# Kernel optimization log

Measured on AMD Instinct MI355X. Metric: run time of the kernel, lower is better.

Reference implementation:

```python
import jax, jax.numpy as jnp
import numpy as np

B, S, D, E, TOPK = 8, 4096, 1024, 64, 2
TEMP = 0.01


def setup_inputs() -> dict:
    key = jax.random.key(0)
    k_x, k_w1, k_b1, k_w2, k_b2 = jax.random.split(key, 5)
    x = jax.random.normal(k_x, (B, S, D), dtype=jnp.float32)
    # torch.nn.Linear default init ~ U(-1/sqrt(fan_in), 1/sqrt(fan_in)); scale ok for reference
    W1 = jax.random.normal(k_w1, (D, 2 * D), dtype=jnp.float32) * (1.0 / np.sqrt(D))
    b1 = jax.random.normal(k_b1, (2 * D,), dtype=jnp.float32) * 0.01
    W2 = jax.random.normal(k_w2, (2 * D, E), dtype=jnp.float32) * (1.0 / np.sqrt(2 * D))
    b2 = jax.random.normal(k_b2, (E,), dtype=jnp.float32) * 0.01
    return {"x": x, "W1": W1, "b1": b1, "W2": W2, "b2": b2}


def reference(x, W1, b1, W2, b2):
    # 2-layer MLP router: [B,S,D] -> [B,S,2D] -> [B,S,E]
    h = jax.nn.relu(jnp.einsum('bsd,df->bsf', x, W1) + b1)
    logits = jnp.einsum('bsf,fe->bse', h, W2) + b2
    # top-k over experts
    top_k_logits, indices = jax.lax.top_k(logits, TOPK)  # [B,S,K]
    # scatter top-k logits into a -inf-filled tensor: equivalent to masking,
    # since scattered values equal logits at those positions
    keep = jax.nn.one_hot(indices, E, dtype=bool).any(axis=-2)  # [B,S,E]
    sparse_logits = jnp.where(keep, logits, -jnp.inf)
    router_output = jax.nn.softmax(sparse_logits, axis=-1)
    ori_router_output = jax.nn.softmax(logits / TEMP, axis=-1)
    return (ori_router_output, router_output, indices)
```

## Files before the change

kernel.cpp:

```cpp
#include <hip/hip_runtime.h>
#include <math.h>
#include <stdint.h>

#define M_TOK 32768
#define D_IN  1024
#define F_HID 2048
#define E_EXP 64

#define O_ORI 0
#define O_RTR (M_TOK * E_EXP)
#define O_IDX (2 * M_TOK * E_EXP)

typedef _Float16 half8 __attribute__((ext_vector_type(8)));
typedef float    f32x4 __attribute__((ext_vector_type(4)));
typedef unsigned int uint32;
typedef uint32   u32x4 __attribute__((ext_vector_type(4)));

#define WS_XH  ((size_t)0)
#define WS_XL  (WS_XH  + (size_t)M_TOK * D_IN * 2)
#define WS_W1H (WS_XL  + (size_t)M_TOK * D_IN * 2)
#define WS_W1L (WS_W1H + (size_t)D_IN * F_HID * 2)
#define WS_W2H (WS_W1L + (size_t)D_IN * F_HID * 2)
#define WS_W2L (WS_W2H + (size_t)F_HID * E_EXP * 2)
#define WS_P   (WS_W2L + (size_t)F_HID * E_EXP * 2)
#define WS_NEED_FULL (WS_P + (size_t)8 * M_TOK * E_EXP * 4)

__device__ __forceinline__ void split_sc(float v, float sc, unsigned short& h, unsigned short& l) {
    const _Float16 hh = (_Float16)v;
    const float hf = (float)hh;
    const _Float16 hs = (_Float16)(hf * sc);
    const _Float16 ls = (_Float16)((v - hf) * sc);
    h = __builtin_bit_cast(unsigned short, hs);
    l = __builtin_bit_cast(unsigned short, ls);
}


__global__ void split_x_k(const float* __restrict__ x,
                          unsigned short* __restrict__ xh, unsigned short* __restrict__ xl) {
    size_t i = ((size_t)blockIdx.x * 256 + threadIdx.x) * 4;
    const float4 v = *(const float4*)&x[i];
    ushort4 h, l;
    split_sc(v.x, 64.f, h.x, l.x); split_sc(v.y, 64.f, h.y, l.y);
    split_sc(v.z, 64.f, h.z, l.z); split_sc(v.w, 64.f, h.w, l.w);
    *(ushort4*)&xh[i] = h;
    *(ushort4*)&xl[i] = l;
}

__global__ void split_w1t_k(const float* __restrict__ W1,
                            unsigned short* __restrict__ wh, unsigned short* __restrict__ wl) {
    __shared__ float t[32][33];
    const int d0 = blockIdx.x * 32;
    const int f0 = blockIdx.y * 32;
    const int r  = threadIdx.x >> 3;
    const int c4 = (threadIdx.x & 7) * 4;
    const float4 v = *(const float4*)&W1[(size_t)(d0 + r) * F_HID + f0 + c4];
    t[r][c4 + 0] = v.x; t[r][c4 + 1] = v.y; t[r][c4 + 2] = v.z; t[r][c4 + 3] = v.w;
    __syncthreads();
    ushort4 h, l;
    split_sc(t[c4 + 0][r], 64.f, h.x, l.x);
    split_sc(t[c4 + 1][r], 64.f, h.y, l.y);
    split_sc(t[c4 + 2][r], 64.f, h.z, l.z);
    split_sc(t[c4 + 3][r], 64.f, h.w, l.w);
    *(ushort4*)&wh[(size_t)(f0 + r) * D_IN + d0 + c4] = h;
    *(ushort4*)&wl[(size_t)(f0 + r) * D_IN + d0 + c4] = l;
}

__global__ void split_w2f_k(const float* __restrict__ W2,
                            unsigned short* __restrict__ wh, unsigned short* __restrict__ wl) {
    const int s  = blockIdx.x;
    const int nt = threadIdx.x >> 6;
    const int l  = threadIdx.x & 63;
    const int fb = s * 32 + (l >> 4) * 8;
    const int e  = nt * 16 + (l & 15);
    unsigned short h[8], lo[8];
#pragma unroll
    for (int j = 0; j < 8; ++j)
        split_sc(W2[(size_t)(fb + j) * E_EXP + e], 16.f, h[j], lo[j]);
    const size_t base = ((size_t)(s * 4 + nt) * 64 + l) * 8;
    ((ushort4*)&wh[base])[0] = make_ushort4(h[0], h[1], h[2], h[3]);
    ((ushort4*)&wh[base])[1] = make_ushort4(h[4], h[5], h[6], h[7]);
    ((ushort4*)&wl[base])[0] = make_ushort4(lo[0], lo[1], lo[2], lo[3]);
    ((ushort4*)&wl[base])[1] = make_ushort4(lo[4], lo[5], lo[6], lo[7]);
}


__device__ __forceinline__ uint32 swz(uint32 o) { return o ^ (((o >> 7) & 7u) << 4); }

#define STAGE16(SRCP, DSTP) \
    __builtin_amdgcn_global_load_lds((const __attribute__((address_space(1))) void*)(SRCP), \
                                     (__attribute__((address_space(3))) void*)(DSTP), 16, 0, 0)


__launch_bounds__(512, 2)
__global__ void gemm1_8w(const unsigned short* __restrict__ xh, const unsigned short* __restrict__ xl,
                         const unsigned short* __restrict__ w1h, const unsigned short* __restrict__ w1l,
                         const unsigned short* __restrict__ w2fh, const unsigned short* __restrict__ w2fl,
                         const float* __restrict__ b1,
                         float* __restrict__ partials)
{
    __shared__ __align__(16) unsigned char lds[131072];

    const int tid  = threadIdx.x;
    const int lane = tid & 63;
    const int w    = tid >> 6;
    const int c15  = lane & 15;
    const int g    = lane >> 4;
    const int wr   = w >> 2;
    const int wc   = w & 3;

    const int bid  = blockIdx.x;
    const int fblk = bid & 7;
    const int mblk = bid >> 3;
    const size_t tok0 = (size_t)mblk * 128;
    const int f0 = fblk * 256;

    uint32 arow, ahalf, brow[2], bhalf[2];
    {
        const uint32 sA = swz((uint32)(tid * 16));
        arow = sA >> 6; ahalf = (sA & 63u) >> 1;
#pragma unroll
        for (int j = 0; j < 2; ++j) {
            const uint32 sB = swz((uint32)(j * 8192 + w * 1024 + lane * 16));
            brow[j] = sB >> 6; bhalf[j] = (sB & 63u) >> 1;
        }
    }

    uint32 offA[4], offB[4];
#pragma unroll
    for (int m = 0; m < 4; ++m)
        offA[m] = swz((uint32)((wr * 64 + m * 16 + c15) * 64 + g * 16));
#pragma unroll
    for (int n = 0; n < 4; ++n)
        offB[n] = swz((uint32)((wc * 64 + n * 16 + c15) * 64 + g * 16));

    f32x4 acc[4][4];
#pragma unroll
    for (int m = 0; m < 4; ++m)
#pragma unroll
        for (int n = 0; n < 4; ++n) acc[m][n] = (f32x4){0.f, 0.f, 0.f, 0.f};

#define STAGE_T(T, BUF) do {                                                         \
    const int d0_ = (T) * 32;                                                        \
    const size_t asrc = (tok0 + arow) * D_IN + (size_t)(d0_ + (int)ahalf);           \
    STAGE16(xh + asrc, lds + (BUF) * 16384 + w * 1024);                              \
    STAGE16(xl + asrc, lds + (BUF) * 16384 + 8192 + w * 1024);                       \
    _Pragma("unroll")                                                                \
    for (int j = 0; j < 2; ++j) {                                                    \
        const size_t bsrc = ((size_t)f0 + brow[j]) * D_IN + (size_t)(d0_ + (int)bhalf[j]); \
        STAGE16(w1h + bsrc, lds + 32768 + (BUF) * 32768 + j * 8192 + w * 1024);      \
        STAGE16(w1l + bsrc, lds + 32768 + (BUF) * 32768 + 16384 + j * 8192 + w * 1024); \
    } } while (0)

    STAGE_T(0, 0);
    STAGE_T(1, 1);

#pragma unroll 1
    for (int t = 0; t < 32; ++t) {
        if (t < 31) asm volatile("s_waitcnt vmcnt(6)" ::: "memory");
        else        asm volatile("s_waitcnt vmcnt(0)" ::: "memory");
        __builtin_amdgcn_s_barrier();
        const unsigned char* Ab = lds + (t & 1) * 16384;
        const unsigned char* Bb = lds + 32768 + (t & 1) * 32768;

        half8 b1f[4], b2f[4];
#pragma unroll
        for (int n = 0; n < 4; ++n) {
            b1f[n] = *(const half8*)(Bb + offB[n]);
            b2f[n] = *(const half8*)(Bb + 16384 + offB[n]);
        }
        half8 a1f[2], a2f[2];
#pragma unroll
        for (int m = 0; m < 2; ++m) {
            a1f[m] = *(const half8*)(Ab + offA[m]);
            a2f[m] = *(const half8*)(Ab + 8192 + offA[m]);
        }
        __builtin_amdgcn_s_setprio(1);
#pragma unroll
        for (int m = 0; m < 2; ++m)
#pragma unroll
            for (int n = 0; n < 4; ++n) {
                acc[m][n] = __builtin_amdgcn_mfma_f32_16x16x32_f16(a1f[m], b1f[n], acc[m][n], 0, 0, 0);
                acc[m][n] = __builtin_amdgcn_mfma_f32_16x16x32_f16(a1f[m], b2f[n], acc[m][n], 0, 0, 0);
                acc[m][n] = __builtin_amdgcn_mfma_f32_16x16x32_f16(a2f[m], b1f[n], acc[m][n], 0, 0, 0);
            }
        __builtin_amdgcn_s_setprio(0);
#pragma unroll
        for (int m = 0; m < 2; ++m) {
            a1f[m] = *(const half8*)(Ab + offA[2 + m]);
            a2f[m] = *(const half8*)(Ab + 8192 + offA[2 + m]);
        }
        __builtin_amdgcn_s_setprio(1);
#pragma unroll
        for (int m = 0; m < 2; ++m)
#pragma unroll
            for (int n = 0; n < 4; ++n) {
                acc[2 + m][n] = __builtin_amdgcn_mfma_f32_16x16x32_f16(a1f[m], b1f[n], acc[2 + m][n], 0, 0, 0);
                acc[2 + m][n] = __builtin_amdgcn_mfma_f32_16x16x32_f16(a1f[m], b2f[n], acc[2 + m][n], 0, 0, 0);
                acc[2 + m][n] = __builtin_amdgcn_mfma_f32_16x16x32_f16(a2f[m], b1f[n], acc[2 + m][n], 0, 0, 0);
            }
        __builtin_amdgcn_s_setprio(0);
        __builtin_amdgcn_s_barrier();
        if (t + 2 < 32) STAGE_T(t + 2, t & 1);
    }
#undef STAGE_T

    {
        float bv[4];
#pragma unroll
        for (int n = 0; n < 4; ++n) bv[n] = b1[f0 + wc * 64 + n * 16 + c15];
#pragma unroll
        for (int m = 0; m < 4; ++m)
#pragma unroll
            for (int n = 0; n < 4; ++n)
#pragma unroll
                for (int r = 0; r < 4; ++r) {
                    float hv = acc[m][n][r] * (1.f / 4096.f) + bv[n];
                    hv = fmaxf(hv, 0.f);
                    const _Float16 hh = (_Float16)hv;
                    const float hf = (float)hh;
                    const _Float16 hsv = (_Float16)(hf * 16.f);
                    const _Float16 lsv = (_Float16)((hv - hf) * 16.f);
                    const uint32 pk = (uint32)__builtin_bit_cast(unsigned short, hsv)
                                    | ((uint32)__builtin_bit_cast(unsigned short, lsv) << 16);
                    const int tok = wr * 64 + m * 16 + g * 4 + r;
                    const int fl  = wc * 64 + n * 16 + c15;
                    *(uint32*)(lds + tok * 1024 + ((fl * 4) ^ ((tok & 15) << 4))) = pk;
                }
    }
    __syncthreads();

    f32x4 acc2[4];
#pragma unroll
    for (int nt = 0; nt < 4; ++nt) acc2[nt] = (f32x4){0.f, 0.f, 0.f, 0.f};

    const int wtok0 = w * 16;
    const int tokA  = wtok0 + c15;
#pragma unroll
    for (int s = 0; s < 8; ++s) {
        const int kf = s * 32 + g * 8;
        const int sg = fblk * 8 + s;
        half8 bf1[4], bf2[4];
#pragma unroll
        for (int nt = 0; nt < 4; ++nt) {
            const size_t base = ((size_t)(sg * 4 + nt) * 64 + lane) * 8;
            bf1[nt] = *(const half8*)&w2fh[base];
            bf2[nt] = *(const half8*)&w2fl[base];
        }
        const u32x4 q0 = *(const u32x4*)(lds + tokA * 1024 + (((kf    ) * 4) ^ (c15 << 4)));
        const u32x4 q1 = *(const u32x4*)(lds + tokA * 1024 + (((kf + 4) * 4) ^ (c15 << 4)));
        u32x4 hi4, lo4;
        hi4[0] = __builtin_amdgcn_perm(q0[1], q0[0], 0x05040100u);
        hi4[1] = __builtin_amdgcn_perm(q0[3], q0[2], 0x05040100u);
        hi4[2] = __builtin_amdgcn_perm(q1[1], q1[0], 0x05040100u);
        hi4[3] = __builtin_amdgcn_perm(q1[3], q1[2], 0x05040100u);
        lo4[0] = __builtin_amdgcn_perm(q0[1], q0[0], 0x07060302u);
        lo4[1] = __builtin_amdgcn_perm(q0[3], q0[2], 0x07060302u);
        lo4[2] = __builtin_amdgcn_perm(q1[1], q1[0], 0x07060302u);
        lo4[3] = __builtin_amdgcn_perm(q1[3], q1[2], 0x07060302u);
        const half8 a1 = __builtin_bit_cast(half8, hi4);
        const half8 a2 = __builtin_bit_cast(half8, lo4);
#pragma unroll
        for (int nt = 0; nt < 4; ++nt) {
            acc2[nt] = __builtin_amdgcn_mfma_f32_16x16x32_f16(a1, bf1[nt], acc2[nt], 0, 0, 0);
            acc2[nt] = __builtin_amdgcn_mfma_f32_16x16x32_f16(a1, bf2[nt], acc2[nt], 0, 0, 0);
            acc2[nt] = __builtin_amdgcn_mfma_f32_16x16x32_f16(a2, bf1[nt], acc2[nt], 0, 0, 0);
        }
    }

    float* pout = partials + ((size_t)fblk * M_TOK + tok0) * E_EXP;
#pragma unroll
    for (int nt = 0; nt < 4; ++nt)
#pragma unroll
        for (int r = 0; r < 4; ++r) {
            const int tl = wtok0 + g * 4 + r;
            pout[(size_t)tl * E_EXP + nt * 16 + c15] = acc2[nt][r] * (1.f / 256.f);
        }
}


__launch_bounds__(256, 4)
__global__ void finalize(const float* __restrict__ partials,
                         const float* __restrict__ b2,
                         float* __restrict__ out)
{
    const int lane = threadIdx.x & 63;
    const int w    = threadIdx.x >> 6;
    const size_t tok0 = (size_t)blockIdx.x * 64;
    const int e = lane;
    const float be = b2[e];

#pragma unroll 1
    for (int i = 0; i < 16; ++i) {
        const size_t tok = tok0 + (size_t)w * 16 + i;
        float l = be;
#pragma unroll
        for (int p = 0; p < 8; ++p)
            l += partials[((size_t)p * M_TOK + tok) * E_EXP + e];

        float v = l; int idx = e;
#pragma unroll
        for (int m = 32; m >= 1; m >>= 1) {
            const float ov = __shfl_xor(v, m, 64);
            const int   oi = __shfl_xor(idx, m, 64);
            if (ov > v || (ov == v && oi < idx)) { v = ov; idx = oi; }
        }
        const float m1 = v; const int i1 = idx;

        v = (e == i1) ? -INFINITY : l; idx = e;
#pragma unroll
        for (int m = 32; m >= 1; m >>= 1) {
            const float ov = __shfl_xor(v, m, 64);
            const int   oi = __shfl_xor(idx, m, 64);
            if (ov > v || (ov == v && oi < idx)) { v = ov; idx = oi; }
        }
        const int i2 = idx;

        const float ex = expf((l - m1) * 100.0f);
        float s = ex;
#pragma unroll
        for (int m = 32; m >= 1; m >>= 1) s += __shfl_xor(s, m, 64);
        const float ori = ex / s;

        const float q = (e == i1 || e == i2) ? expf(l - m1) : 0.f;
        float s2 = q;
#pragma unroll
        for (int m = 32; m >= 1; m >>= 1) s2 += __shfl_xor(s2, m, 64);
        const float rtr = q / s2;

        out[O_ORI + tok * E_EXP + e] = ori;
        out[O_RTR + tok * E_EXP + e] = rtr;
        if (e == 0) {
            out[O_IDX + tok * 2 + 0] = (float)i1;
            out[O_IDX + tok * 2 + 1] = (float)i2;
        }
    }
}


#define BT  64
#define NB  256

__launch_bounds__(256, 2)
__global__ void router_mfma(const unsigned short* __restrict__ xh, const unsigned short* __restrict__ xl,
                            const unsigned short* __restrict__ w1h, const unsigned short* __restrict__ w1l,
                            const unsigned short* __restrict__ w2fh, const unsigned short* __restrict__ w2fl,
                            const float* __restrict__ b1, const float* __restrict__ b2,
                            float* __restrict__ out)
{
    __shared__ __align__(16) unsigned char xs_h[BT * 64];
    __shared__ __align__(16) unsigned char xs_l[BT * 64];
    __shared__ __align__(16) unsigned char w1s_h[NB * 64];
    __shared__ __align__(16) unsigned char w1s_l[NB * 64];
    __shared__ __align__(16) unsigned char hsbuf[BT * 132 * 4];

    const int tid  = threadIdx.x;
    const int lane = tid & 63;
    const int w    = tid >> 6;
    const int c15  = lane & 15;
    const int g    = lane >> 4;
    const size_t tok0 = (size_t)blockIdx.x * BT;

    uint32* hs = (uint32*)hsbuf;
    float*  ls = (float*)hsbuf;

    f32x4 acc2h[4], acc2x[4];
#pragma unroll
    for (int nt = 0; nt < 4; ++nt) {
        acc2h[nt] = (f32x4){0.f, 0.f, 0.f, 0.f};
        acc2x[nt] = (f32x4){0.f, 0.f, 0.f, 0.f};
    }

    const uint32 kqb = (uint32)g * 16u;

    for (int fc = 0; fc < F_HID; fc += NB) {
        f32x4 ahh[4][4], axx[4][4];
#pragma unroll
        for (int mt = 0; mt < 4; ++mt)
#pragma unroll
            for (int nt = 0; nt < 4; ++nt) {
                ahh[mt][nt] = (f32x4){0.f, 0.f, 0.f, 0.f};
                axx[mt][nt] = (f32x4){0.f, 0.f, 0.f, 0.f};
            }

        for (int d0 = 0; d0 < D_IN; d0 += 32) {
            __syncthreads();
            {
                uint32 o = (uint32)w * 1024u + (uint32)lane * 16u;
                uint32 s = swz(o);
                uint32 r = s >> 6, hb = (s & 63u) >> 1;
                const unsigned short* sp;
                sp = xh + (tok0 + r) * D_IN + (size_t)(d0 + (int)hb);
                STAGE16(sp, xs_h + (size_t)w * 1024);
                sp = xl + (tok0 + r) * D_IN + (size_t)(d0 + (int)hb);
                STAGE16(sp, xs_l + (size_t)w * 1024);
#pragma unroll
                for (int q = 0; q < 4; ++q) {
                    const uint32 c_ = (uint32)(q * 4 + w);
                    uint32 o2 = c_ * 1024u + (uint32)lane * 16u;
                    uint32 s2 = swz(o2);
                    uint32 r2 = s2 >> 6, hb2 = (s2 & 63u) >> 1;
                    sp = w1h + ((size_t)(fc + (int)r2)) * D_IN + (size_t)(d0 + (int)hb2);
                    STAGE16(sp, w1s_h + (size_t)c_ * 1024);
                    sp = w1l + ((size_t)(fc + (int)r2)) * D_IN + (size_t)(d0 + (int)hb2);
                    STAGE16(sp, w1s_l + (size_t)c_ * 1024);
                }
            }
            __syncthreads();

            half8 ah[4], al[4], bh[4], bl[4];
#pragma unroll
            for (int mt = 0; mt < 4; ++mt) {
                const uint32 off = swz((uint32)(mt * 16 + c15) * 64u + kqb);
                ah[mt] = *(const half8*)(xs_h + off);
                al[mt] = *(const half8*)(xs_l + off);
            }
#pragma unroll
            for (int nt = 0; nt < 4; ++nt) {
                const uint32 row = (uint32)(w * 64 + nt * 16 + c15);
                const uint32 off = swz(row * 64u + kqb);
                bh[nt] = *(const half8*)(w1s_h + off);
                bl[nt] = *(const half8*)(w1s_l + off);
            }
#pragma unroll
            for (int mt = 0; mt < 4; ++mt)
#pragma unroll
                for (int nt = 0; nt < 4; ++nt) {
                    ahh[mt][nt] = __builtin_amdgcn_mfma_f32_16x16x32_f16(ah[mt], bh[nt], ahh[mt][nt], 0, 0, 0);
                    axx[mt][nt] = __builtin_amdgcn_mfma_f32_16x16x32_f16(ah[mt], bl[nt], axx[mt][nt], 0, 0, 0);
                    axx[mt][nt] = __builtin_amdgcn_mfma_f32_16x16x32_f16(al[mt], bh[nt], axx[mt][nt], 0, 0, 0);
                }
        }

        const int fl0 = (w & 1) * 64;
#pragma unroll
        for (int phase = 0; phase < 2; ++phase) {
            if ((w >> 1) == phase) {
#pragma unroll
                for (int nt = 0; nt < 4; ++nt) {
                    const float b1v = b1[fc + w * 64 + nt * 16 + c15];
#pragma unroll
                    for (int mt = 0; mt < 4; ++mt) {
#pragma unroll
                        for (int r = 0; r < 4; ++r) {
                            float hv = (ahh[mt][nt][r] + axx[mt][nt][r]) * (1.f / 4096.f) + b1v;
                            hv = fmaxf(hv, 0.f);
                            const _Float16 hhv0 = (_Float16)hv;
                            const float hf = (float)hhv0;
                            const _Float16 hhv = (_Float16)(hf * 16.f);
                            const _Float16 hlv = (_Float16)((hv - hf) * 16.f);
                            uint32 pk = (uint32)__builtin_bit_cast(unsigned short, hhv)
                                      | ((uint32)__builtin_bit_cast(unsigned short, hlv) << 16);
                            const int t = mt * 16 + g * 4 + r;
                            hs[t * 132 + fl0 + nt * 16 + c15] = pk;
                        }
                    }
                }
            }
            __syncthreads();
            const int tA = w * 16 + c15;
#pragma unroll
            for (int ktl = 0; ktl < 4; ++ktl) {
                const u32x4 q0 = *(const u32x4*)&hs[tA * 132 + ktl * 32 + g * 8];
                const u32x4 q1 = *(const u32x4*)&hs[tA * 132 + ktl * 32 + g * 8 + 4];
                u32x4 hi4, lo4;
                hi4[0] = __builtin_amdgcn_perm(q0[1], q0[0], 0x05040100u);
                hi4[1] = __builtin_amdgcn_perm(q0[3], q0[2], 0x05040100u);
                hi4[2] = __builtin_amdgcn_perm(q1[1], q1[0], 0x05040100u);
                hi4[3] = __builtin_amdgcn_perm(q1[3], q1[2], 0x05040100u);
                lo4[0] = __builtin_amdgcn_perm(q0[1], q0[0], 0x07060302u);
                lo4[1] = __builtin_amdgcn_perm(q0[3], q0[2], 0x07060302u);
                lo4[2] = __builtin_amdgcn_perm(q1[1], q1[0], 0x07060302u);
                lo4[3] = __builtin_amdgcn_perm(q1[3], q1[2], 0x07060302u);
                const half8 a_h = __builtin_bit_cast(half8, hi4);
                const half8 a_l = __builtin_bit_cast(half8, lo4);
                const int sg = (fc >> 5) + phase * 4 + ktl;
#pragma unroll
                for (int nt = 0; nt < 4; ++nt) {
                    const size_t base = ((size_t)(sg * 4 + nt) * 64 + lane) * 8;
                    const half8 b_h = *(const half8*)&w2fh[base];
                    const half8 b_l = *(const half8*)&w2fl[base];
                    acc2h[nt] = __builtin_amdgcn_mfma_f32_16x16x32_f16(a_h, b_h, acc2h[nt], 0, 0, 0);
                    acc2x[nt] = __builtin_amdgcn_mfma_f32_16x16x32_f16(a_h, b_l, acc2x[nt], 0, 0, 0);
                    acc2x[nt] = __builtin_amdgcn_mfma_f32_16x16x32_f16(a_l, b_h, acc2x[nt], 0, 0, 0);
                }
            }
            __syncthreads();
        }
    }

#pragma unroll
    for (int nt = 0; nt < 4; ++nt)
#pragma unroll
        for (int r = 0; r < 4; ++r) {
            const int t = w * 16 + g * 4 + r;
            ls[t * 68 + nt * 16 + c15] = (acc2h[nt][r] + acc2x[nt][r]) * (1.f / 256.f);
        }
    __syncthreads();

    const int e = lane;
    const float be = b2[e];
#pragma unroll 1
    for (int i = 0; i < 16; ++i) {
        const float l = ls[(w * 16 + i) * 68 + e] + be;

        float v = l; int idx = e;
#pragma unroll
        for (int m = 32; m >= 1; m >>= 1) {
            const float ov = __shfl_xor(v, m, 64);
            const int   oi = __shfl_xor(idx, m, 64);
            if (ov > v || (ov == v && oi < idx)) { v = ov; idx = oi; }
        }
        const float m1 = v; const int i1 = idx;

        v = (e == i1) ? -INFINITY : l; idx = e;
#pragma unroll
        for (int m = 32; m >= 1; m >>= 1) {
            const float ov = __shfl_xor(v, m, 64);
            const int   oi = __shfl_xor(idx, m, 64);
            if (ov > v || (ov == v && oi < idx)) { v = ov; idx = oi; }
        }
        const int i2 = idx;

        const float ex = expf((l - m1) * 100.0f);
        float s = ex;
#pragma unroll
        for (int m = 32; m >= 1; m >>= 1) s += __shfl_xor(s, m, 64);
        const float ori = ex / s;

        const float q = (e == i1 || e == i2) ? expf(l - m1) : 0.f;
        float s2 = q;
#pragma unroll
        for (int m = 32; m >= 1; m >>= 1) s2 += __shfl_xor(s2, m, 64);
        const float rtr = q / s2;

        const size_t tok = tok0 + (size_t)w * 16 + i;
        out[O_ORI + tok * E_EXP + e] = ori;
        out[O_RTR + tok * E_EXP + e] = rtr;
        if (e == 0) {
            out[O_IDX + tok * 2 + 0] = (float)i1;
            out[O_IDX + tok * 2 + 1] = (float)i2;
        }
    }
}


extern "C" void kernel_launch(void* const* d_in, const int* in_sizes, int n_in,
                              void* d_out, int out_size, void* d_ws, size_t ws_size,
                              hipStream_t stream) {
    const float* x  = (const float*)d_in[0];
    const float* W1 = (const float*)d_in[1];
    const float* b1 = (const float*)d_in[2];
    const float* W2 = (const float*)d_in[3];
    const float* b2 = (const float*)d_in[4];
    float* out = (float*)d_out;

    unsigned char* ws = (unsigned char*)d_ws;
    unsigned short* xh  = (unsigned short*)(ws + WS_XH);
    unsigned short* xl  = (unsigned short*)(ws + WS_XL);
    unsigned short* w1h = (unsigned short*)(ws + WS_W1H);
    unsigned short* w1l = (unsigned short*)(ws + WS_W1L);
    unsigned short* w2h = (unsigned short*)(ws + WS_W2H);
    unsigned short* w2l = (unsigned short*)(ws + WS_W2L);
    float*          parts = (float*)(ws + WS_P);

    hipLaunchKernelGGL(split_x_k,  dim3(M_TOK * D_IN / 4 / 256), dim3(256), 0, stream, x, xh, xl);
    hipLaunchKernelGGL(split_w1t_k, dim3(D_IN / 32, F_HID / 32), dim3(256), 0, stream, W1, w1h, w1l);
    hipLaunchKernelGGL(split_w2f_k, dim3(F_HID / 32), dim3(256), 0, stream, W2, w2h, w2l);

    if (ws_size >= WS_NEED_FULL) {
        hipLaunchKernelGGL(gemm1_8w, dim3(2048), dim3(512), 0, stream,
                           xh, xl, w1h, w1l, w2h, w2l, b1, parts);
        hipLaunchKernelGGL(finalize, dim3(M_TOK / 64), dim3(256), 0, stream, parts, b2, out);
    } else {
        hipLaunchKernelGGL(router_mfma, dim3(M_TOK / BT), dim3(256), 0, stream,
                           xh, xl, w1h, w1l, w2h, w2l, b1, b2, out);
    }
}
```

Before: 524.3 us.

## Fuse both router GEMMs and the softmax finalize into one kernel

Each block now owns 128 tokens and loops over all eight 256-wide hidden chunks. For each chunk it runs the first GEMM, writes the ReLU hidden tile into LDS, and accumulates the second GEMM in registers. The top-k and softmax epilogue then runs in the same kernel from an LDS logits tile. This removes the 8-way partial-logit buffer in global memory (a large write and read) and the separate finalize launch. The cost is a grid of only 256 large blocks, with the hidden-tile conversion and second GEMM serialized inside each block between chunks, which limits latency hiding.

```diff
diff --git a/kernel.cpp b/kernel.cpp
--- a/kernel.cpp
+++ b/kernel.cpp
@@ -22,8 +22,7 @@
 #define WS_W1L (WS_W1H + (size_t)D_IN * F_HID * 2)
 #define WS_W2H (WS_W1L + (size_t)D_IN * F_HID * 2)
 #define WS_W2L (WS_W2H + (size_t)F_HID * E_EXP * 2)
-#define WS_P   (WS_W2L + (size_t)F_HID * E_EXP * 2)
-#define WS_NEED_FULL (WS_P + (size_t)8 * M_TOK * E_EXP * 4)
+#define WS_NEED (WS_W2L + (size_t)F_HID * E_EXP * 2)
 
 __device__ __forceinline__ void split_sc(float v, float sc, unsigned short& h, unsigned short& l) {
     const _Float16 hh = (_Float16)v;
@@ -92,11 +91,11 @@
 
 
 __launch_bounds__(512, 2)
-__global__ void gemm1_8w(const unsigned short* __restrict__ xh, const unsigned short* __restrict__ xl,
-                         const unsigned short* __restrict__ w1h, const unsigned short* __restrict__ w1l,
-                         const unsigned short* __restrict__ w2fh, const unsigned short* __restrict__ w2fl,
-                         const float* __restrict__ b1,
-                         float* __restrict__ partials)
+__global__ void router_one(const unsigned short* __restrict__ xh, const unsigned short* __restrict__ xl,
+                           const unsigned short* __restrict__ w1h, const unsigned short* __restrict__ w1l,
+                           const unsigned short* __restrict__ w2fh, const unsigned short* __restrict__ w2fl,
+                           const float* __restrict__ b1, const float* __restrict__ b2,
+                           float* __restrict__ out)
 {
     __shared__ __align__(16) unsigned char lds[131072];
 
@@ -108,11 +107,7 @@
     const int wr   = w >> 2;
     const int wc   = w & 3;
 
-    const int bid  = blockIdx.x;
-    const int fblk = bid & 7;
-    const int mblk = bid >> 3;
-    const size_t tok0 = (size_t)mblk * 128;
-    const int f0 = fblk * 256;
+    const size_t tok0 = (size_t)blockIdx.x * 128;
 
     uint32 arow, ahalf, brow[2], bhalf[2];
     {
@@ -133,169 +128,161 @@
     for (int n = 0; n < 4; ++n)
         offB[n] = swz((uint32)((wc * 64 + n * 16 + c15) * 64 + g * 16));
 
-    f32x4 acc[4][4];
-#pragma unroll
-    for (int m = 0; m < 4; ++m)
-#pragma unroll
-        for (int n = 0; n < 4; ++n) acc[m][n] = (f32x4){0.f, 0.f, 0.f, 0.f};
-
-#define STAGE_T(T, BUF) do {                                                         \
+    f32x4 acc2[4];
+#pragma unroll
+    for (int nt = 0; nt < 4; ++nt) acc2[nt] = (f32x4){0.f, 0.f, 0.f, 0.f};
+
+#define STAGE_T(T, BUF, F0) do {                                                     \
     const int d0_ = (T) * 32;                                                        \
     const size_t asrc = (tok0 + arow) * D_IN + (size_t)(d0_ + (int)ahalf);           \
     STAGE16(xh + asrc, lds + (BUF) * 16384 + w * 1024);                              \
     STAGE16(xl + asrc, lds + (BUF) * 16384 + 8192 + w * 1024);                       \
     _Pragma("unroll")                                                                \
     for (int j = 0; j < 2; ++j) {                                                    \
-        const size_t bsrc = ((size_t)f0 + brow[j]) * D_IN + (size_t)(d0_ + (int)bhalf[j]); \
+        const size_t bsrc = ((size_t)(F0) + brow[j]) * D_IN + (size_t)(d0_ + (int)bhalf[j]); \
         STAGE16(w1h + bsrc, lds + 32768 + (BUF) * 32768 + j * 8192 + w * 1024);      \
         STAGE16(w1l + bsrc, lds + 32768 + (BUF) * 32768 + 16384 + j * 8192 + w * 1024); \
     } } while (0)
 
-    STAGE_T(0, 0);
-    STAGE_T(1, 1);
-
 #pragma unroll 1
-    for (int t = 0; t < 32; ++t) {
-        if (t < 31) asm volatile("s_waitcnt vmcnt(6)" ::: "memory");
-        else        asm volatile("s_waitcnt vmcnt(0)" ::: "memory");
-        __builtin_amdgcn_s_barrier();
-        const unsigned char* Ab = lds + (t & 1) * 16384;
-        const unsigned char* Bb = lds + 32768 + (t & 1) * 32768;
-
-        half8 b1f[4], b2f[4];
-#pragma unroll
-        for (int n = 0; n < 4; ++n) {
-            b1f[n] = *(const half8*)(Bb + offB[n]);
-            b2f[n] = *(const half8*)(Bb + 16384 + offB[n]);
-        }
-        half8 a1f[2], a2f[2];
-#pragma unroll
-        for (int m = 0; m < 2; ++m) {
-            a1f[m] = *(const half8*)(Ab + offA[m]);
-            a2f[m] = *(const half8*)(Ab + 8192 + offA[m]);
-        }
-        __builtin_amdgcn_s_setprio(1);
-#pragma unroll
-        for (int m = 0; m < 2; ++m)
+    for (int fc = 0; fc < F_HID; fc += 256) {
+        f32x4 acc[4][4];
+#pragma unroll
+        for (int m = 0; m < 4; ++m)
+#pragma unroll
+            for (int n = 0; n < 4; ++n) acc[m][n] = (f32x4){0.f, 0.f, 0.f, 0.f};
+
+        __syncthreads();
+        STAGE_T(0, 0, fc);
+        STAGE_T(1, 1, fc);
+
+#pragma unroll 1
+        for (int t = 0; t < 32; ++t) {
+            if (t < 31) asm volatile("s_waitcnt vmcnt(6)" ::: "memory");
+            else        asm volatile("s_waitcnt vmcnt(0)" ::: "memory");
+            __builtin_amdgcn_s_barrier();
+            const unsigned char* Ab = lds + (t & 1) * 16384;
+            const unsigned char* Bb = lds + 32768 + (t & 1) * 32768;
+
+            half8 b1f[4], b2f[4];
 #pragma unroll
             for (int n = 0; n < 4; ++n) {
-                acc[m][n] = __builtin_amdgcn_mfma_f32_16x16x32_f16(a1f[m], b1f[n], acc[m][n], 0, 0, 0);
-                acc[m][n] = __builtin_amdgcn_mfma_f32_16x16x32_f16(a1f[m], b2f[n], acc[m][n], 0, 0, 0);
-                acc[m][n] = __builtin_amdgcn_mfma_f32_16x16x32_f16(a2f[m], b1f[n], acc[m][n], 0, 0, 0);
-            }
-        __builtin_amdgcn_s_setprio(0);
-#pragma unroll
-        for (int m = 0; m < 2; ++m) {
-            a1f[m] = *(const half8*)(Ab + offA[2 + m]);
-            a2f[m] = *(const half8*)(Ab + 8192 + offA[2 + m]);
-        }
-        __builtin_amdgcn_s_setprio(1);
-#pragma unroll
-        for (int m = 0; m < 2; ++m)
-#pragma unroll
-            for (int n = 0; n < 4; ++n) {
-                acc[2 + m][n] = __builtin_amdgcn_mfma_f32_16x16x32_f16(a1f[m], b1f[n], acc[2 + m][n], 0, 0, 0);
-                acc[2 + m][n] = __builtin_amdgcn_mfma_f32_16x16x32_f16(a1f[m], b2f[n], acc[2 + m][n], 0, 0, 0);
-                acc[2 + m][n] = __builtin_amdgcn_mfma_f32_16x16x32_f16(a2f[m], b1f[n], acc[2 + m][n], 0, 0, 0);
-            }
-        __builtin_amdgcn_s_setprio(0);
-        __builtin_amdgcn_s_barrier();
-        if (t + 2 < 32) STAGE_T(t + 2, t & 1);
+                b1f[n] = *(const half8*)(Bb + offB[n]);
+                b2f[n] = *(const half8*)(Bb + 16384 + offB[n]);
+            }
+            half8 a1f[2], a2f[2];
+#pragma unroll
+            for (int m = 0; m < 2; ++m) {
+                a1f[m] = *(const half8*)(Ab + offA[m]);
+                a2f[m] = *(const half8*)(Ab + 8192 + offA[m]);
+            }
+            __builtin_amdgcn_s_setprio(1);
+#pragma unroll
+            for (int m = 0; m < 2; ++m)
+#pragma unroll
+                for (int n = 0; n < 4; ++n) {
+                    acc[m][n] = __builtin_amdgcn_mfma_f32_16x16x32_f16(a1f[m], b1f[n], acc[m][n], 0, 0, 0);
+                    acc[m][n] = __builtin_amdgcn_mfma_f32_16x16x32_f16(a1f[m], b2f[n], acc[m][n], 0, 0, 0);
+                    acc[m][n] = __builtin_amdgcn_mfma_f32_16x16x32_f16(a2f[m], b1f[n], acc[m][n], 0, 0, 0);
+                }
+            __builtin_amdgcn_s_setprio(0);
+#pragma unroll
+            for (int m = 0; m < 2; ++m) {
+                a1f[m] = *(const half8*)(Ab + offA[2 + m]);
+                a2f[m] = *(const half8*)(Ab + 8192 + offA[2 + m]);
+            }
+            __builtin_amdgcn_s_setprio(1);
+#pragma unroll
+            for (int m = 0; m < 2; ++m)
+#pragma unroll
+                for (int n = 0; n < 4; ++n) {
+                    acc[2 + m][n] = __builtin_amdgcn_mfma_f32_16x16x32_f16(a1f[m], b1f[n], acc[2 + m][n], 0, 0, 0);
+                    acc[2 + m][n] = __builtin_amdgcn_mfma_f32_16x16x32_f16(a1f[m], b2f[n], acc[2 + m][n], 0, 0, 0);
+                    acc[2 + m][n] = __builtin_amdgcn_mfma_f32_16x16x32_f16(a2f[m], b1f[n], acc[2 + m][n], 0, 0, 0);
+                }
+            __builtin_amdgcn_s_setprio(0);
+            __builtin_amdgcn_s_barrier();
+            if (t + 2 < 32) STAGE_T(t + 2, t & 1, fc);
+        }
+
+        {
+            float bv[4];
+#pragma unroll
+            for (int n = 0; n < 4; ++n) bv[n] = b1[fc + wc * 64 + n * 16 + c15];
+#pragma unroll
+            for (int m = 0; m < 4; ++m)
+#pragma unroll
+                for (int n = 0; n < 4; ++n)
+#pragma unroll
+                    for (int r = 0; r < 4; ++r) {
+                        float hv = acc[m][n][r] * (1.f / 4096.f) + bv[n];
+                        hv = fmaxf(hv, 0.f);
+                        const _Float16 hh = (_Float16)hv;
+                        const float hf = (float)hh;
+                        const _Float16 hsv = (_Float16)(hf * 16.f);
+                        const _Float16 lsv = (_Float16)((hv - hf) * 16.f);
+                        const uint32 pk = (uint32)__builtin_bit_cast(unsigned short, hsv)
+                                        | ((uint32)__builtin_bit_cast(unsigned short, lsv) << 16);
+                        const int tok = wr * 64 + m * 16 + g * 4 + r;
+                        const int fl  = wc * 64 + n * 16 + c15;
+                        *(uint32*)(lds + tok * 1024 + ((fl * 4) ^ ((tok & 15) << 4))) = pk;
+                    }
+        }
+        __syncthreads();
+
+        {
+            const int tokA = w * 16 + c15;
+#pragma unroll
+            for (int s = 0; s < 8; ++s) {
+                const int kf = s * 32 + g * 8;
+                const int sg = (fc >> 5) + s;
+                half8 bf1[4], bf2[4];
+#pragma unroll
+                for (int nt = 0; nt < 4; ++nt) {
+                    const size_t base = ((size_t)(sg * 4 + nt) * 64 + lane) * 8;
+                    bf1[nt] = *(const half8*)&w2fh[base];
+                    bf2[nt] = *(const half8*)&w2fl[base];
+                }
+                const u32x4 q0 = *(const u32x4*)(lds + tokA * 1024 + (((kf    ) * 4) ^ (c15 << 4)));
+                const u32x4 q1 = *(const u32x4*)(lds + tokA * 1024 + (((kf + 4) * 4) ^ (c15 << 4)));
+                u32x4 hi4, lo4;
+                hi4[0] = __builtin_amdgcn_perm(q0[1], q0[0], 0x05040100u);
+                hi4[1] = __builtin_amdgcn_perm(q0[3], q0[2], 0x05040100u);
+                hi4[2] = __builtin_amdgcn_perm(q1[1], q1[0], 0x05040100u);
+                hi4[3] = __builtin_amdgcn_perm(q1[3], q1[2], 0x05040100u);
+                lo4[0] = __builtin_amdgcn_perm(q0[1], q0[0], 0x07060302u);
+                lo4[1] = __builtin_amdgcn_perm(q0[3], q0[2], 0x07060302u);
+                lo4[2] = __builtin_amdgcn_perm(q1[1], q1[0], 0x07060302u);
+                lo4[3] = __builtin_amdgcn_perm(q1[3], q1[2], 0x07060302u);
+                const half8 a1 = __builtin_bit_cast(half8, hi4);
+                const half8 a2 = __builtin_bit_cast(half8, lo4);
+#pragma unroll
+                for (int nt = 0; nt < 4; ++nt) {
+                    acc2[nt] = __builtin_amdgcn_mfma_f32_16x16x32_f16(a1, bf1[nt], acc2[nt], 0, 0, 0);
+                    acc2[nt] = __builtin_amdgcn_mfma_f32_16x16x32_f16(a1, bf2[nt], acc2[nt], 0, 0, 0);
+                    acc2[nt] = __builtin_amdgcn_mfma_f32_16x16x32_f16(a2, bf1[nt], acc2[nt], 0, 0, 0);
+                }
+            }
+        }
     }
 #undef STAGE_T
 
-    {
-        float bv[4];
-#pragma unroll
-        for (int n = 0; n < 4; ++n) bv[n] = b1[f0 + wc * 64 + n * 16 + c15];
-#pragma unroll
-        for (int m = 0; m < 4; ++m)
-#pragma unroll
-            for (int n = 0; n < 4; ++n)
-#pragma unroll
-                for (int r = 0; r < 4; ++r) {
-                    float hv = acc[m][n][r] * (1.f / 4096.f) + bv[n];
-                    hv = fmaxf(hv, 0.f);
-                    const _Float16 hh = (_Float16)hv;
-                    const float hf = (float)hh;
-                    const _Float16 hsv = (_Float16)(hf * 16.f);
-                    const _Float16 lsv = (_Float16)((hv - hf) * 16.f);
-                    const uint32 pk = (uint32)__builtin_bit_cast(unsigned short, hsv)
-                                    | ((uint32)__builtin_bit_cast(unsigned short, lsv) << 16);
-                    const int tok = wr * 64 + m * 16 + g * 4 + r;
-                    const int fl  = wc * 64 + n * 16 + c15;
-                    *(uint32*)(lds + tok * 1024 + ((fl * 4) ^ ((tok & 15) << 4))) = pk;
-                }
-    }
     __syncthreads();
-
-    f32x4 acc2[4];
-#pragma unroll
-    for (int nt = 0; nt < 4; ++nt) acc2[nt] = (f32x4){0.f, 0.f, 0.f, 0.f};
-
-    const int wtok0 = w * 16;
-    const int tokA  = wtok0 + c15;
-#pragma unroll
-    for (int s = 0; s < 8; ++s) {
-        const int kf = s * 32 + g * 8;
-        const int sg = fblk * 8 + s;
-        half8 bf1[4], bf2[4];
-#pragma unroll
-        for (int nt = 0; nt < 4; ++nt) {
-            const size_t base = ((size_t)(sg * 4 + nt) * 64 + lane) * 8;
-            bf1[nt] = *(const half8*)&w2fh[base];
-            bf2[nt] = *(const half8*)&w2fl[base];
-        }
-        const u32x4 q0 = *(const u32x4*)(lds + tokA * 1024 + (((kf    ) * 4) ^ (c15 << 4)));
-        const u32x4 q1 = *(const u32x4*)(lds + tokA * 1024 + (((kf + 4) * 4) ^ (c15 << 4)));
-        u32x4 hi4, lo4;
-        hi4[0] = __builtin_amdgcn_perm(q0[1], q0[0], 0x05040100u);
-        hi4[1] = __builtin_amdgcn_perm(q0[3], q0[2], 0x05040100u);
-        hi4[2] = __builtin_amdgcn_perm(q1[1], q1[0], 0x05040100u);
-        hi4[3] = __builtin_amdgcn_perm(q1[3], q1[2], 0x05040100u);
-        lo4[0] = __builtin_amdgcn_perm(q0[1], q0[0], 0x07060302u);
-        lo4[1] = __builtin_amdgcn_perm(q0[3], q0[2], 0x07060302u);
-        lo4[2] = __builtin_amdgcn_perm(q1[1], q1[0], 0x07060302u);
-        lo4[3] = __builtin_amdgcn_perm(q1[3], q1[2], 0x07060302u);
-        const half8 a1 = __builtin_bit_cast(half8, hi4);
-        const half8 a2 = __builtin_bit_cast(half8, lo4);
-#pragma unroll
-        for (int nt = 0; nt < 4; ++nt) {
-            acc2[nt] = __builtin_amdgcn_mfma_f32_16x16x32_f16(a1, bf1[nt], acc2[nt], 0, 0, 0);
-            acc2[nt] = __builtin_amdgcn_mfma_f32_16x16x32_f16(a1, bf2[nt], acc2[nt], 0, 0, 0);
-            acc2[nt] = __builtin_amdgcn_mfma_f32_16x16x32_f16(a2, bf1[nt], acc2[nt], 0, 0, 0);
-        }
-    }
-
-    float* pout = partials + ((size_t)fblk * M_TOK + tok0) * E_EXP;
+    float* ls = (float*)lds;
 #pragma unroll
     for (int nt = 0; nt < 4; ++nt)
 #pragma unroll
         for (int r = 0; r < 4; ++r) {
-            const int tl = wtok0 + g * 4 + r;
-            pout[(size_t)tl * E_EXP + nt * 16 + c15] = acc2[nt][r] * (1.f / 256.f);
-        }
-}
-
-
-__launch_bounds__(256, 4)
-__global__ void finalize(const float* __restrict__ partials,
-                         const float* __restrict__ b2,
-                         float* __restrict__ out)
-{
-    const int lane = threadIdx.x & 63;
-    const int w    = threadIdx.x >> 6;
-    const size_t tok0 = (size_t)blockIdx.x * 64;
+            const int tl = w * 16 + g * 4 + r;
+            ls[tl * 68 + nt * 16 + c15] = acc2[nt][r] * (1.f / 256.f);
+        }
+    __syncthreads();
+
     const int e = lane;
     const float be = b2[e];
-
 #pragma unroll 1
     for (int i = 0; i < 16; ++i) {
-        const size_t tok = tok0 + (size_t)w * 16 + i;
-        float l = be;
-#pragma unroll
-        for (int p = 0; p < 8; ++p)
-            l += partials[((size_t)p * M_TOK + tok) * E_EXP + e];
+        const float l = ls[(w * 16 + i) * 68 + e] + be;
 
         float v = l; int idx = e;
 #pragma unroll
@@ -327,6 +314,7 @@
         for (int m = 32; m >= 1; m >>= 1) s2 += __shfl_xor(s2, m, 64);
         const float rtr = q / s2;
 
+        const size_t tok = tok0 + (size_t)w * 16 + i;
         out[O_ORI + tok * E_EXP + e] = ori;
         out[O_RTR + tok * E_EXP + e] = rtr;
         if (e == 0) {
@@ -561,16 +549,14 @@
     unsigned short* w1l = (unsigned short*)(ws + WS_W1L);
     unsigned short* w2h = (unsigned short*)(ws + WS_W2H);
     unsigned short* w2l = (unsigned short*)(ws + WS_W2L);
-    float*          parts = (float*)(ws + WS_P);
 
     hipLaunchKernelGGL(split_x_k,  dim3(M_TOK * D_IN / 4 / 256), dim3(256), 0, stream, x, xh, xl);
     hipLaunchKernelGGL(split_w1t_k, dim3(D_IN / 32, F_HID / 32), dim3(256), 0, stream, W1, w1h, w1l);
     hipLaunchKernelGGL(split_w2f_k, dim3(F_HID / 32), dim3(256), 0, stream, W2, w2h, w2l);
 
-    if (ws_size >= WS_NEED_FULL) {
-        hipLaunchKernelGGL(gemm1_8w, dim3(2048), dim3(512), 0, stream,
-                           xh, xl, w1h, w1l, w2h, w2l, b1, parts);
-        hipLaunchKernelGGL(finalize, dim3(M_TOK / 64), dim3(256), 0, stream, parts, b2, out);
+    if (ws_size >= WS_NEED) {
+        hipLaunchKernelGGL(router_one, dim3(M_TOK / 128), dim3(512), 0, stream,
+                           xh, xl, w1h, w1l, w2h, w2l, b1, b2, out);
     } else {
         hipLaunchKernelGGL(router_mfma, dim3(M_TOK / BT), dim3(256), 0, stream,
                            xh, xl, w1h, w1l, w2h, w2l, b1, b2, out);
```

Measured after the change: 504.9 us. -3.7%, faster.
